# Optimization experiments

Hardware: AMD Instinct MI355X
Metric: run time of the kernel (lower is better)

## Reference

```python
import jax, jax.numpy as jnp
import numpy as np

NEG_INF = -1e30  # stand-in for float('-inf') that is softmax-safe


def setup_inputs() -> dict:
    key = jax.random.key(0)
    ks = jax.random.split(key, 6)
    B, H, S, D = 2, 8, 1024, 64
    NF, K = 4, 3
    return {
        "query": jax.random.normal(ks[0], (B, H, S, D), dtype=jnp.float32),
        "keys": jax.random.normal(ks[1], (B, H, S, D), dtype=jnp.float32),
        "vals": jax.random.normal(ks[2], (B, H, S, D), dtype=jnp.float32),
        "mask": jnp.ones((B, 1, S, S), dtype=jnp.int32),
        "conv_w": jax.random.normal(ks[3], (NF, 1, K, K), dtype=jnp.float32) * (1.0 / K),
        "conv_b": jnp.zeros((NF,), dtype=jnp.float32),
        "lin_w": jax.random.normal(ks[4], (1, NF), dtype=jnp.float32) * 0.5,
        "lin_b": jnp.zeros((1,), dtype=jnp.float32),
    }


def reference(query, keys, vals, mask, conv_w, conv_b, lin_w, lin_b):
    B, H, S, D = query.shape
    NF = conv_w.shape[0]
    K = conv_w.shape[2]
    scale = jnp.asarray(D, query.dtype) ** 0.5

    # [B,H,S,S] raw dot-product scores
    dp = jnp.einsum("bhsd,bhtd->bhst", query, keys) / scale

    # conv2d over the score matrix: treat (B*H) as batch, 1 input channel
    x = dp.reshape(B * H, 1, S, S)
    conv = jax.lax.conv_general_dilated(
        x, conv_w,
        window_strides=(1, 1),
        padding=[(K // 2, K // 2), (K // 2, K // 2)],
        dimension_numbers=("NCHW", "OIHW", "NCHW"),
    ) + conv_b[None, :, None, None]
    conv = jax.nn.leaky_relu(conv, negative_slope=0.01)  # [B*H, NF, S, S]

    # per-pixel linear over the filter axis (Linear(num_filters, 1))
    conv = conv.reshape(B, H, NF, S, S)
    preattn = jnp.einsum("bhfst,f->bhst", conv, lin_w[0]) + lin_b[0]

    # masking + softmax (mask broadcasts over heads)
    preattn = jnp.where(mask == 0, jnp.asarray(NEG_INF, preattn.dtype), preattn)
    attn = jax.nn.softmax(preattn, axis=-1)

    # dropout is identity in eval mode
    return jnp.einsum("bhst,bhtd->bhsd", attn, vals)
```

## Files before the change

kernel.cpp:

```cpp
#include <hip/hip_runtime.h>
#include <math.h>

#define S_LEN 1024
#define D_DIM 64
#define NBH   16
#define RPB   14
#define NSB   74

typedef unsigned short ushort_t;
typedef unsigned int uint_t;
typedef __attribute__((ext_vector_type(8))) _Float16 half8;
typedef __attribute__((ext_vector_type(2))) _Float16 h2;
typedef __attribute__((ext_vector_type(4))) short short4v;
typedef __attribute__((ext_vector_type(4))) float f32x4;
typedef __attribute__((ext_vector_type(2))) float f32x2;

__device__ __forceinline__ ushort_t f16bits(float x) {
    _Float16 h = (_Float16)x;
    ushort_t b;
    __builtin_memcpy(&b, &h, 2);
    return b;
}
__device__ __forceinline__ h2 as_h2(uint_t u) {
    h2 r;
    __builtin_memcpy(&r, &u, 4);
    return r;
}

__global__ __launch_bounds__(256) void prep(
    const float* __restrict__ k, const float* __restrict__ v,
    const int* __restrict__ mask,
    ushort_t* __restrict__ kh, ushort_t* __restrict__ vh,
    unsigned* __restrict__ mw)
{
    __shared__ float Ls[64][65];
    const int tid = threadIdx.x;
    const int bx = blockIdx.x;
    if (bx < 512) {
        const int gid  = bx * 256 + tid;
        const int bh   = gid >> 13;
        const int tile = (gid >> 7) & 63;
        const int ch   = (gid >> 6) & 1;
        const int lane = gid & 63;
        const int quad = lane >> 4, t15 = lane & 15;
        const float* src = k + ((size_t)bh * S_LEN + tile * 16 + t15) * D_DIM
                             + ch * 32 + quad * 8;
        float x[8];
        *(float4*)(x + 0) = *(const float4*)(src);
        *(float4*)(x + 4) = *(const float4*)(src + 4);
        ushort_t hv[8];
        #pragma unroll
        for (int i = 0; i < 8; ++i) hv[i] = f16bits(x[i]);
        *(short4v*)(kh + (size_t)gid * 8)     = *(short4v*)(hv);
        *(short4v*)(kh + (size_t)gid * 8 + 4) = *(short4v*)(hv + 4);
    } else if (bx < 768) {
        const int bi = bx - 512;
        const int tt = bi & 15, bh = bi >> 4;
        const float* vb = v + ((size_t)bh * S_LEN + tt * 64) * D_DIM;
        #pragma unroll
        for (int p = 0; p < 4; ++p) {
            int idx = p * 1024 + tid * 4;
            int r = idx >> 6, c = idx & 63;
            float4 x = *(const float4*)(vb + r * 64 + c);
            Ls[r][c] = x.x; Ls[r][c+1] = x.y; Ls[r][c+2] = x.z; Ls[r][c+3] = x.w;
        }
        __syncthreads();
        const int d = tid >> 2, c0 = (tid & 3) * 16;
        ushort_t hi[16];
        #pragma unroll
        for (int j = 0; j < 16; ++j) hi[j] = f16bits(Ls[c0 + j][d]);
        const int tb0 = tt * 8 + (c0 >> 3);
        const size_t o0 = (((size_t)bh * 128 + tb0) * 64 + d) * 8;
        const size_t o1 = (((size_t)bh * 128 + tb0 + 1) * 64 + d) * 8;
        *(short4v*)(vh + o0)     = *(short4v*)(hi);
        *(short4v*)(vh + o0 + 4) = *(short4v*)(hi + 4);
        *(short4v*)(vh + o1)     = *(short4v*)(hi + 8);
        *(short4v*)(vh + o1 + 4) = *(short4v*)(hi + 12);
    } else {
        const int gid = (bx - 768) * 256 + tid;
        const int row = gid >> 5, wd = gid & 31;
        const int4* mp = (const int4*)(mask + (size_t)row * 1024 + wd * 32);
        unsigned bits = 0;
        #pragma unroll
        for (int p = 0; p < 8; ++p) {
            int4 qv = mp[p];
            bits |= (qv.x != 0 ? 1u : 0u) << (p * 4 + 0);
            bits |= (qv.y != 0 ? 1u : 0u) << (p * 4 + 1);
            bits |= (qv.z != 0 ? 1u : 0u) << (p * 4 + 2);
            bits |= (qv.w != 0 ? 1u : 0u) << (p * 4 + 3);
        }
        mw[(size_t)row * 32 + wd] = bits;
    }
}

#define DPSTR 1040
__global__ __launch_bounds__(512) void fused_qk_conv_av(
    const float* __restrict__ q,
    const ushort_t* __restrict__ kh, const unsigned* __restrict__ mw,
    const ushort_t* __restrict__ vh,
    const float* __restrict__ conv_w, const float* __restrict__ conv_b,
    const float* __restrict__ lin_w, const float* __restrict__ lin_b,
    float* __restrict__ out)
{
    __shared__ ushort_t dpH[16 * DPSTR];
    __shared__ float oBuf[16][68];
    __shared__ float lsPart[16][4];
    __shared__ unsigned mb[16][32];

    const int st = blockIdx.x, bh = blockIdx.y;
    const int s0 = st * RPB;
    const int b  = bh >> 3;
    const int tid = threadIdx.x;
    const int wave = tid >> 6, lane = tid & 63;
    const int m = lane & 15, quad = lane >> 4;

    {
        const int o = tid >> 5, wd = tid & 31;
        const int s = s0 - 1 + o;
        mb[o][wd] = (s >= 0 && s < S_LEN)
                  ? mw[((size_t)b * S_LEN + s) * 32 + wd] : 0u;
    }
    if (tid < 64) {
        const int row = tid >> 2, i = tid & 3;
        const int idx = (i < 2) ? i : 1024 + i;
        dpH[row * DPSTR + idx] = 0;
    }

    const int sA = s0 - 1 + m;
    const int sQ = sA < 0 ? 0 : (sA > S_LEN - 1 ? S_LEN - 1 : sA);
    const float* qp = q + ((size_t)bh * S_LEN + sQ) * D_DIM + quad * 8;
    float qa[16];
    *(float4*)(qa + 0)  = *(const float4*)(qp + 0);
    *(float4*)(qa + 4)  = *(const float4*)(qp + 4);
    *(float4*)(qa + 8)  = *(const float4*)(qp + 32);
    *(float4*)(qa + 12) = *(const float4*)(qp + 36);
    half8 AH0, AH1;
    #pragma unroll
    for (int i = 0; i < 8; ++i) {
        AH0[i] = (_Float16)(qa[i] * 0.125f);
        AH1[i] = (_Float16)(qa[8 + i] * 0.125f);
    }

    #pragma unroll
    for (int tt = 0; tt < 8; ++tt) {
        const int tile = wave * 8 + tt;
        const size_t kb = (((size_t)bh * 64 + tile) * 128 + lane) * 8;
        half8 KH0 = *(const half8*)(kh + kb);
        half8 KH1 = *(const half8*)(kh + kb + 512);
        f32x4 a = {0.f, 0.f, 0.f, 0.f};
        a = __builtin_amdgcn_mfma_f32_16x16x32_f16(AH0, KH0, a, 0, 0, 0);
        a = __builtin_amdgcn_mfma_f32_16x16x32_f16(AH1, KH1, a, 0, 0, 0);
        const int col = tile * 16 + m;
        #pragma unroll
        for (int r = 0; r < 4; ++r) {
            const int row = quad * 4 + r;
            const int s = s0 - 1 + row;
            const float v = (s >= 0 && s < S_LEN) ? a[r] : 0.f;
            dpH[row * DPSTR + col + 2] = f16bits(v);
        }
    }

    float w[36];
    #pragma unroll
    for (int i = 0; i < 36; ++i) w[i] = conv_w[i];
    float cb[4], lw[4];
    #pragma unroll
    for (int f = 0; f < 4; ++f) { cb[f] = conv_b[f]; lw[f] = lin_w[f]; }
    const float lb = lin_b[0];
    const f32x2 zero2 = {0.f, 0.f};
    const f32x2 c001  = {0.01f, 0.01f};

    __syncthreads();

    const int rh = tid >> 8, cg = tid & 255, c0 = cg * 4;
    uint2 Ps[8];
    #pragma unroll
    for (int pass = 0; pass < 2; ++pass) {
        const int obase = rh * 8 + pass * 4;
        float rowv[6][6];
        #pragma unroll
        for (int jj = 0; jj < 6; ++jj) {
            const int dr = obase - 1 + jj;
            if (dr >= 0 && dr < 16) {
                const ushort_t* rp = &dpH[dr * DPSTR + c0];
                uint2 r0 = *(const uint2*)rp;
                uint2 r1 = *(const uint2*)(rp + 4);
                h2 pA = as_h2(r0.x), pB = as_h2(r0.y);
                h2 pC = as_h2(r1.x), pD = as_h2(r1.y);
                rowv[jj][0] = (float)pA[1];
                rowv[jj][1] = (float)pB[0]; rowv[jj][2] = (float)pB[1];
                rowv[jj][3] = (float)pC[0]; rowv[jj][4] = (float)pC[1];
                rowv[jj][5] = (float)pD[0];
            } else {
                #pragma unroll
                for (int i = 0; i < 6; ++i) rowv[jj][i] = 0.f;
            }
        }
        float ls[4];
        #pragma unroll
        for (int jo = 0; jo < 4; ++jo) {
            const int o = obase + jo;
            const bool act = (o >= 1) && (o <= RPB) && (s0 - 1 + o < S_LEN);
            if (act) {
                f32x2 pa = {lb, lb}, pb = {lb, lb};
                #pragma unroll
                for (int f = 0; f < 4; ++f) {
                    f32x2 ca = {cb[f], cb[f]}, cbv = ca;
                    #pragma unroll
                    for (int dr = 0; dr < 3; ++dr) {
                        const float* vv = rowv[jo + dr];
                        #pragma unroll
                        for (int dc = 0; dc < 3; ++dc) {
                            const float wt = w[f * 9 + dr * 3 + dc];
                            const f32x2 wt2 = {wt, wt};
                            f32x2 ia = {vv[dc],     vv[dc + 1]};
                            f32x2 ib = {vv[dc + 2], vv[dc + 3]};
                            ca  = __builtin_elementwise_fma(wt2, ia, ca);
                            cbv = __builtin_elementwise_fma(wt2, ib, cbv);
                        }
                    }
                    const f32x2 lwv = {lw[f], lw[f]};
                    f32x2 la  = __builtin_elementwise_fma(
                        c001, __builtin_elementwise_min(ca, zero2),
                        __builtin_elementwise_max(ca, zero2));
                    f32x2 lb2 = __builtin_elementwise_fma(
                        c001, __builtin_elementwise_min(cbv, zero2),
                        __builtin_elementwise_max(cbv, zero2));
                    pa = __builtin_elementwise_fma(lwv, la, pa);
                    pb = __builtin_elementwise_fma(lwv, lb2, pb);
                }
                const unsigned word = mb[o][cg >> 3];
                const unsigned nib  = (word >> ((cg & 7) * 4)) & 0xFu;
                float pre[4] = {pa.x, pa.y, pb.x, pb.y};
                #pragma unroll
                for (int i = 0; i < 4; ++i)
                    if (!((nib >> i) & 1u)) pre[i] = -1e30f;
                float pv[4];
                #pragma unroll
                for (int i = 0; i < 4; ++i) pv[i] = __expf(pre[i]);
                ls[jo] = (pv[0] + pv[1]) + (pv[2] + pv[3]);
                Ps[pass * 4 + jo].x =
                    (uint_t)f16bits(pv[0]) | ((uint_t)f16bits(pv[1]) << 16);
                Ps[pass * 4 + jo].y =
                    (uint_t)f16bits(pv[2]) | ((uint_t)f16bits(pv[3]) << 16);
            } else {
                Ps[pass * 4 + jo].x = 0u;
                Ps[pass * 4 + jo].y = 0u;
                ls[jo] = 0.f;
            }
        }
        #pragma unroll
        for (int jo = 0; jo < 4; ++jo) {
            float t = ls[jo];
            #pragma unroll
            for (int off = 1; off < 64; off <<= 1) t += __shfl_xor(t, off);
            if (lane == 0) lsPart[obase + jo][wave & 3] = t;
        }
    }
    __syncthreads();

    #pragma unroll
    for (int i = 0; i < 8; ++i) {
        const int o = rh * 8 + i;
        *(uint2*)&dpH[o * DPSTR + c0] = Ps[i];
    }
    __syncthreads();

    const int d0 = (wave & 3) * 16;
    const int th = wave >> 2;
    f32x4 O = {0.f, 0.f, 0.f, 0.f};
    #pragma unroll 4
    for (int i = 0; i < 16; ++i) {
        const int c = th * 16 + i;
        half8 ph = *(const half8*)&dpH[m * DPSTR + c * 32 + quad * 8];
        const size_t vb = (((size_t)bh * 128 + c * 4 + quad) * 64 + d0 + m) * 8;
        half8 vv = *(const half8*)(vh + vb);
        O = __builtin_amdgcn_mfma_f32_16x16x32_f16(ph, vv, O, 0, 0, 0);
    }
    if (wave < 4) {
        #pragma unroll
        for (int r = 0; r < 4; ++r) oBuf[quad * 4 + r][d0 + m] = O[r];
    }
    __syncthreads();
    if (wave >= 4) {
        #pragma unroll
        for (int r = 0; r < 4; ++r) {
            const int br = quad * 4 + r;
            const int s = s0 - 1 + br;
            if (br >= 1 && br <= RPB && s < S_LEN) {
                const float lsum = (lsPart[br][0] + lsPart[br][1]) +
                                   (lsPart[br][2] + lsPart[br][3]);
                out[((size_t)bh * S_LEN + s) * D_DIM + d0 + m] =
                    (O[r] + oBuf[br][d0 + m]) / lsum;
            }
        }
    }
}

extern "C" void kernel_launch(void* const* d_in, const int* in_sizes, int n_in,
                              void* d_out, int out_size, void* d_ws, size_t ws_size,
                              hipStream_t stream) {
    const float* q      = (const float*)d_in[0];
    const float* k      = (const float*)d_in[1];
    const float* v      = (const float*)d_in[2];
    const int*   mask   = (const int*)d_in[3];
    const float* conv_w = (const float*)d_in[4];
    const float* conv_b = (const float*)d_in[5];
    const float* lin_w  = (const float*)d_in[6];
    const float* lin_b  = (const float*)d_in[7];
    float* out = (float*)d_out;

    char* wsb = (char*)d_ws;
    const size_t MB = 1024 * 1024;
    ushort_t* kh = (ushort_t*)(wsb + 0 * MB);
    ushort_t* vh = (ushort_t*)(wsb + 2 * MB);
    unsigned* mw = (unsigned*)(wsb + 4 * MB);

    prep<<<dim3(1024), 256, 0, stream>>>(k, v, mask, kh, vh, mw);
    fused_qk_conv_av<<<dim3(NSB, NBH), 512, 0, stream>>>(
        q, kh, mw, vh, conv_w, conv_b, lin_w, lin_b, out);
}
```

Before: 120.7 us.

## Fold scale into K prep, use abs-form leaky relu, MFMA row sums

Moves the 1/sqrt(D) scale from the per-block Q conversion into the K conversion in the prep kernel. Rewrites leaky_relu combined with the linear weight as a*y + b*|y| with log2e folded in, so the softmax numerator can use exp2 directly. Replaces the per-row shuffle reductions of the softmax sum with an extra MFMA against a ones vector in the PV loop. Together these drop the wave-level shuffle reductions and some ALU work, at the cost of doubling the MFMA count in the PV loop and computing the row sum from the f16-rounded probabilities.

After: 117.3 us. 2.9% less time.

```diff
diff --git a/kernel.cpp b/kernel.cpp
--- a/kernel.cpp
+++ b/kernel.cpp
@@ -13,7 +13,6 @@
 typedef __attribute__((ext_vector_type(2))) _Float16 h2;
 typedef __attribute__((ext_vector_type(4))) short short4v;
 typedef __attribute__((ext_vector_type(4))) float f32x4;
-typedef __attribute__((ext_vector_type(2))) float f32x2;
 
 __device__ __forceinline__ ushort_t f16bits(float x) {
     _Float16 h = (_Float16)x;
@@ -25,6 +24,16 @@
     h2 r;
     __builtin_memcpy(&r, &u, 4);
     return r;
+}
+__device__ __forceinline__ float uniform_f(float x) {
+    return __int_as_float(__builtin_amdgcn_readfirstlane(__float_as_int(x)));
+}
+__device__ __forceinline__ float fast_exp2(float x) {
+#if __has_builtin(__builtin_amdgcn_exp2f)
+    return __builtin_amdgcn_exp2f(x);
+#else
+    return exp2f(x);
+#endif
 }
 
 __global__ __launch_bounds__(256) void prep(
@@ -50,7 +59,7 @@
         *(float4*)(x + 4) = *(const float4*)(src + 4);
         ushort_t hv[8];
         #pragma unroll
-        for (int i = 0; i < 8; ++i) hv[i] = f16bits(x[i]);
+        for (int i = 0; i < 8; ++i) hv[i] = f16bits(x[i] * 0.125f);
         *(short4v*)(kh + (size_t)gid * 8)     = *(short4v*)(hv);
         *(short4v*)(kh + (size_t)gid * 8 + 4) = *(short4v*)(hv + 4);
     } else if (bx < 768) {
@@ -104,7 +113,7 @@
 {
     __shared__ ushort_t dpH[16 * DPSTR];
     __shared__ float oBuf[16][68];
-    __shared__ float lsPart[16][4];
+    __shared__ float lsRow[16];
     __shared__ unsigned mb[16][32];
 
     const int st = blockIdx.x, bh = blockIdx.y;
@@ -137,8 +146,8 @@
     half8 AH0, AH1;
     #pragma unroll
     for (int i = 0; i < 8; ++i) {
-        AH0[i] = (_Float16)(qa[i] * 0.125f);
-        AH1[i] = (_Float16)(qa[8 + i] * 0.125f);
+        AH0[i] = (_Float16)qa[i];
+        AH1[i] = (_Float16)qa[8 + i];
     }
 
     #pragma unroll
@@ -163,12 +172,16 @@
     float w[36];
     #pragma unroll
     for (int i = 0; i < 36; ++i) w[i] = conv_w[i];
-    float cb[4], lw[4];
-    #pragma unroll
-    for (int f = 0; f < 4; ++f) { cb[f] = conv_b[f]; lw[f] = lin_w[f]; }
-    const float lb = lin_b[0];
-    const f32x2 zero2 = {0.f, 0.f};
-    const f32x2 c001  = {0.01f, 0.01f};
+    const float L2E = 1.44269504088896341f;
+    float cb[4], aF[4], bF[4];
+    #pragma unroll
+    for (int f = 0; f < 4; ++f) {
+        cb[f] = conv_b[f];
+        const float lwf = lin_w[f];
+        aF[f] = uniform_f(0.505f * lwf * L2E);
+        bF[f] = uniform_f(0.495f * lwf * L2E);
+    }
+    const float lbE = uniform_f(lin_b[0] * L2E);
 
     __syncthreads();
 
@@ -177,7 +190,7 @@
     #pragma unroll
     for (int pass = 0; pass < 2; ++pass) {
         const int obase = rh * 8 + pass * 4;
-        float rowv[6][6];
+        float xv[6][6];
         #pragma unroll
         for (int jj = 0; jj < 6; ++jj) {
             const int dr = obase - 1 + jj;
@@ -187,58 +200,52 @@
                 uint2 r1 = *(const uint2*)(rp + 4);
                 h2 pA = as_h2(r0.x), pB = as_h2(r0.y);
                 h2 pC = as_h2(r1.x), pD = as_h2(r1.y);
-                rowv[jj][0] = (float)pA[1];
-                rowv[jj][1] = (float)pB[0]; rowv[jj][2] = (float)pB[1];
-                rowv[jj][3] = (float)pC[0]; rowv[jj][4] = (float)pC[1];
-                rowv[jj][5] = (float)pD[0];
+                xv[jj][0] = (float)pA[1];
+                xv[jj][1] = (float)pB[0]; xv[jj][2] = (float)pB[1];
+                xv[jj][3] = (float)pC[0]; xv[jj][4] = (float)pC[1];
+                xv[jj][5] = (float)pD[0];
             } else {
                 #pragma unroll
-                for (int i = 0; i < 6; ++i) rowv[jj][i] = 0.f;
+                for (int i = 0; i < 6; ++i) xv[jj][i] = 0.f;
             }
         }
-        float ls[4];
         #pragma unroll
         for (int jo = 0; jo < 4; ++jo) {
             const int o = obase + jo;
             const bool act = (o >= 1) && (o <= RPB) && (s0 - 1 + o < S_LEN);
             if (act) {
-                f32x2 pa = {lb, lb}, pb = {lb, lb};
+                float pr[4] = {lbE, lbE, lbE, lbE};
                 #pragma unroll
                 for (int f = 0; f < 4; ++f) {
-                    f32x2 ca = {cb[f], cb[f]}, cbv = ca;
+                    const float* wf = w + f * 9;
+                    float acc[4];
+                    const float w00 = wf[0];
                     #pragma unroll
-                    for (int dr = 0; dr < 3; ++dr) {
-                        const float* vv = rowv[jo + dr];
+                    for (int c = 0; c < 4; ++c) acc[c] = w00 * xv[jo][c];
+                    #pragma unroll
+                    for (int t = 1; t < 9; ++t) {
+                        const int dr = t / 3, dc = t % 3;
+                        const float wt = wf[t];
                         #pragma unroll
-                        for (int dc = 0; dc < 3; ++dc) {
-                            const float wt = w[f * 9 + dr * 3 + dc];
-                            const f32x2 wt2 = {wt, wt};
-                            f32x2 ia = {vv[dc],     vv[dc + 1]};
-                            f32x2 ib = {vv[dc + 2], vv[dc + 3]};
-                            ca  = __builtin_elementwise_fma(wt2, ia, ca);
-                            cbv = __builtin_elementwise_fma(wt2, ib, cbv);
-                        }
+                        for (int c = 0; c < 4; ++c)
+                            acc[c] = fmaf(wt, xv[jo + dr][dc + c], acc[c]);
                     }
-                    const f32x2 lwv = {lw[f], lw[f]};
-                    f32x2 la  = __builtin_elementwise_fma(
-                        c001, __builtin_elementwise_min(ca, zero2),
-                        __builtin_elementwise_max(ca, zero2));
-                    f32x2 lb2 = __builtin_elementwise_fma(
-                        c001, __builtin_elementwise_min(cbv, zero2),
-                        __builtin_elementwise_max(cbv, zero2));
-                    pa = __builtin_elementwise_fma(lwv, la, pa);
-                    pb = __builtin_elementwise_fma(lwv, lb2, pb);
+                    const float cbf = cb[f], af = aF[f], bf = bF[f];
+                    #pragma unroll
+                    for (int c = 0; c < 4; ++c) {
+                        const float y = acc[c] + cbf;
+                        pr[c] = fmaf(af, y, pr[c]);
+                        pr[c] = fmaf(bf, fabsf(y), pr[c]);
+                    }
                 }
                 const unsigned word = mb[o][cg >> 3];
                 const unsigned nib  = (word >> ((cg & 7) * 4)) & 0xFu;
-                float pre[4] = {pa.x, pa.y, pb.x, pb.y};
-                #pragma unroll
-                for (int i = 0; i < 4; ++i)
-                    if (!((nib >> i) & 1u)) pre[i] = -1e30f;
                 float pv[4];
                 #pragma unroll
-                for (int i = 0; i < 4; ++i) pv[i] = __expf(pre[i]);
-                ls[jo] = (pv[0] + pv[1]) + (pv[2] + pv[3]);
+                for (int c = 0; c < 4; ++c) {
+                    const float pe = ((nib >> c) & 1u) ? pr[c] : -1e30f;
+                    pv[c] = fast_exp2(pe);
+                }
                 Ps[pass * 4 + jo].x =
                     (uint_t)f16bits(pv[0]) | ((uint_t)f16bits(pv[1]) << 16);
                 Ps[pass * 4 + jo].y =
@@ -246,15 +253,7 @@
             } else {
                 Ps[pass * 4 + jo].x = 0u;
                 Ps[pass * 4 + jo].y = 0u;
-                ls[jo] = 0.f;
             }
-        }
-        #pragma unroll
-        for (int jo = 0; jo < 4; ++jo) {
-            float t = ls[jo];
-            #pragma unroll
-            for (int off = 1; off < 64; off <<= 1) t += __shfl_xor(t, off);
-            if (lane == 0) lsPart[obase + jo][wave & 3] = t;
         }
     }
     __syncthreads();
@@ -268,18 +267,29 @@
 
     const int d0 = (wave & 3) * 16;
     const int th = wave >> 2;
-    f32x4 O = {0.f, 0.f, 0.f, 0.f};
+    f32x4 O  = {0.f, 0.f, 0.f, 0.f};
+    f32x4 RS = {0.f, 0.f, 0.f, 0.f};
+    half8 ONE;
+    #pragma unroll
+    for (int i = 0; i < 8; ++i) ONE[i] = (_Float16)1.0f;
+    const ushort_t* ph_base = &dpH[m * DPSTR + th * 512 + quad * 8];
+    const ushort_t* vv_base = vh + ((size_t)bh * 65536
+                                    + (size_t)(th * 64 + quad) * 512
+                                    + (size_t)(d0 + m) * 8);
     #pragma unroll 4
     for (int i = 0; i < 16; ++i) {
-        const int c = th * 16 + i;
-        half8 ph = *(const half8*)&dpH[m * DPSTR + c * 32 + quad * 8];
-        const size_t vb = (((size_t)bh * 128 + c * 4 + quad) * 64 + d0 + m) * 8;
-        half8 vv = *(const half8*)(vh + vb);
-        O = __builtin_amdgcn_mfma_f32_16x16x32_f16(ph, vv, O, 0, 0, 0);
+        half8 ph = *(const half8*)(ph_base + i * 32);
+        half8 vv = *(const half8*)(vv_base + (size_t)i * 2048);
+        O  = __builtin_amdgcn_mfma_f32_16x16x32_f16(ph, vv, O, 0, 0, 0);
+        RS = __builtin_amdgcn_mfma_f32_16x16x32_f16(ph, ONE, RS, 0, 0, 0);
     }
     if (wave < 4) {
         #pragma unroll
         for (int r = 0; r < 4; ++r) oBuf[quad * 4 + r][d0 + m] = O[r];
+    }
+    if (wave == 0 && m == 0) {
+        #pragma unroll
+        for (int r = 0; r < 4; ++r) lsRow[quad * 4 + r] = RS[r];
     }
     __syncthreads();
     if (wave >= 4) {
@@ -288,8 +298,7 @@
             const int br = quad * 4 + r;
             const int s = s0 - 1 + br;
             if (br >= 1 && br <= RPB && s < S_LEN) {
-                const float lsum = (lsPart[br][0] + lsPart[br][1]) +
-                                   (lsPart[br][2] + lsPart[br][3]);
+                const float lsum = lsRow[br] + RS[r];
                 out[((size_t)bh * S_LEN + s) * D_DIM + d0 + m] =
                     (O[r] + oBuf[br][d0 + m]) / lsum;
             }
```
